# Kernel tuning notes

Measured on AMD Instinct MI355X. Metric: run time of the kernel, lower is better.

The kernel has to match this reference:

```python
import jax, jax.numpy as jnp
import numpy as np

X_CH, Y_CH, DIM, NUM_HEAD = 256, 512, 128, 4
H_DIM = DIM // NUM_HEAD
GAMMA = H_DIM ** (-0.5)


def conv1x1(x, w, b):
    # x: [B,C,H,W], w: [O,C], b: [O]
    return jnp.einsum('bchw,oc->bohw', x, w) + b[None, :, None, None]


def _split_qkv(qkv, bs, hw):
    # qkv: [B, 3*DIM, H, W] -> q,k,v each [B, NUM_HEAD, HW, H_DIM]
    qkv = qkv.reshape(bs, 3, NUM_HEAD, H_DIM, hw)
    qkv = jnp.transpose(qkv, (1, 0, 2, 4, 3))  # [3, B, H, HW, D]
    return qkv[0], qkv[1], qkv[2]


def setup_inputs() -> dict:
    key = jax.random.key(0)
    ks = jax.random.split(key, 12)
    s = lambda fan_in: 1.0 / np.sqrt(fan_in)
    x = jax.random.normal(ks[0], (2, X_CH, 64, 64), dtype=jnp.float32)
    y = jax.random.normal(ks[1], (2, Y_CH, 32, 32), dtype=jnp.float32)
    wx_qkv = jax.random.normal(ks[2], (3 * DIM, X_CH), dtype=jnp.float32) * s(X_CH)
    bx_qkv = jax.random.normal(ks[3], (3 * DIM,), dtype=jnp.float32) * s(X_CH)
    wy_qkv = jax.random.normal(ks[4], (3 * DIM, Y_CH), dtype=jnp.float32) * s(Y_CH)
    by_qkv = jax.random.normal(ks[5], (3 * DIM,), dtype=jnp.float32) * s(Y_CH)
    wpx = jax.random.normal(ks[6], (X_CH, DIM), dtype=jnp.float32) * s(DIM)
    bpx = jax.random.normal(ks[7], (X_CH,), dtype=jnp.float32) * s(DIM)
    wpy = jax.random.normal(ks[8], (Y_CH, DIM), dtype=jnp.float32) * s(DIM)
    bpy = jax.random.normal(ks[9], (Y_CH,), dtype=jnp.float32) * s(DIM)
    return {"x": x, "y": y, "wx_qkv": wx_qkv, "bx_qkv": bx_qkv,
            "wy_qkv": wy_qkv, "by_qkv": by_qkv,
            "wpx": wpx, "bpx": bpx, "wpy": wpy, "bpy": bpy}


def reference(x, y, wx_qkv, bx_qkv, wy_qkv, by_qkv, wpx, bpx, wpy, bpy):
    bs, _, h_x, w_x = x.shape
    _, _, h_y, w_y = y.shape
    hw_x, hw_y = h_x * w_x, h_y * w_y

    q_x, k_x, v_x = _split_qkv(conv1x1(x, wx_qkv, bx_qkv), bs, hw_x)
    q_y, k_y, v_y = _split_qkv(conv1x1(y, wy_qkv, by_qkv), bs, hw_y)

    # x attends to y
    atten_x = jax.nn.softmax(jnp.einsum('bhqd,bhkd->bhqk', q_x, k_y) * GAMMA, axis=-1)
    out_x = jnp.einsum('bhqk,bhkd->bhqd', atten_x, v_y)  # [B,H,HWx,D]
    out_x = jnp.transpose(out_x, (0, 1, 3, 2)).reshape(bs, DIM, h_x, w_x)

    # y attends to x
    atten_y = jax.nn.softmax(jnp.einsum('bhqd,bhkd->bhqk', q_y, k_x) * GAMMA, axis=-1)
    out_y = jnp.einsum('bhqk,bhkd->bhqd', atten_y, v_x)
    out_y = jnp.transpose(out_y, (0, 1, 3, 2)).reshape(bs, DIM, h_y, w_y)

    out_x = conv1x1(out_x, wpx, bpx) + x
    out_y = conv1x1(out_y, wpy, bpy) + y
    return out_x, out_y
```

## Files before the change

### kernel.cpp

```cpp
#include <hip/hip_runtime.h>
#include <hip/hip_bf16.h>
#include <cstdint>

#define B 2
#define NH 4
#define HD 32
#define DIM 128
#define CX 256
#define CY 512
#define PX 4096
#define PY 1024
#define QKV 384
#define GAMMA 0.17677669529663687f

typedef unsigned short u16;
typedef unsigned int u32;

using short8 = __attribute__((ext_vector_type(8))) short;
using f32x4  = __attribute__((ext_vector_type(4))) float;

__device__ __forceinline__ float bf2f(u32 h) {
  union { u32 u; float f; } v; v.u = (h & 0xffffu) << 16; return v.f;
}
__device__ __forceinline__ u16 f2bf(float f) {
  u32 u = __float_as_uint(f);
  u32 r = (u + 0x7fffu + ((u >> 16) & 1u)) >> 16;
  return (u16)r;
}
__device__ __forceinline__ void gl_lds16(const u16* g, u16* l) {
  __builtin_amdgcn_global_load_lds(
      (const __attribute__((address_space(1))) void*)g,
      (__attribute__((address_space(3))) void*)l, 16, 0, 0);
}
__device__ __forceinline__ bool is_f32(const void* src) {
  u32 u = ((const u16*)src)[2 * (threadIdx.x & 63)];
  return __ballot((u & 0x7F80u) >= 0x4600u) != 0ull;
}

#define N_X   (B * CX * PX)
#define N_Y   (B * CY * PY)
#define N_WX  (QKV * CX)
#define N_BX  (QKV)
#define N_WY  (QKV * CY)
#define N_BY  (QKV)
#define N_WPX (CX * DIM)
#define N_BPX (CX)
#define N_WPY (CY * DIM)
#define N_BPY (CY)

enum : size_t {
  OFF_CWX   = 0,
  OFF_CBX   = OFF_CWX  + N_WX,
  OFF_CWY   = OFF_CBX  + N_BX,
  OFF_CBY   = OFF_CWY  + N_WY,
  OFF_CWPX  = OFF_CBY  + N_BY,
  OFF_CBPX  = OFF_CWPX + N_WPX,
  OFF_CWPY  = OFF_CBPX + N_BPX,
  OFF_CBPY  = OFF_CWPY + N_WPY,
  OFF_XT    = OFF_CBPY + N_BPY,
  OFF_YT    = OFF_XT   + (size_t)B * PX * CX,
  OFF_QPX   = OFF_YT   + (size_t)B * PY * CY,
  OFF_KPX   = OFF_QPX  + (size_t)B * NH * PX * HD,
  OFF_QPY   = OFF_KPX  + (size_t)B * NH * PX * HD,
  OFF_KPY   = OFF_QPY  + (size_t)B * NH * PY * HD,
  OFF_VCX   = OFF_KPY  + (size_t)B * NH * PY * HD,
  OFF_VCY   = OFF_VCX  + (size_t)B * DIM * PX,
  OFF_OTX   = OFF_VCY  + (size_t)B * DIM * PY,
  OFF_OTY   = OFF_OTX  + (size_t)B * PX * DIM,
  WS_END    = OFF_OTY  + (size_t)B * PY * DIM,
};

#define XPX_BLKS 2048
#define XPY_BLKS 1024
__global__ __launch_bounds__(256) void k_prep(
    const void* x, const void* y, const void* wx, const void* bx,
    const void* wy, const void* by, const void* wpx, const void* bpx,
    const void* wpy, const void* bpy, u16* __restrict__ ws) {
  const int id = blockIdx.x;
  if (id < XPX_BLKS + XPY_BLKS) {
    __shared__ u16 tile[32][33];
    const void* src; u16* dst; int C, P, p_t, c_t, b;
    if (id < XPX_BLKS) {
      src = x; dst = ws + OFF_XT; C = CX; P = PX;
      p_t = id & 127; c_t = (id >> 7) & 7; b = id >> 10;
    } else {
      int id2 = id - XPX_BLKS;
      src = y; dst = ws + OFF_YT; C = CY; P = PY;
      p_t = id2 & 31; c_t = (id2 >> 5) & 15; b = id2 >> 9;
    }
    const bool f32in = is_f32(src);
    const int tx = threadIdx.x & 31, ty = threadIdx.x >> 5;
    const int p0 = p_t * 32, c0 = c_t * 32;
#pragma unroll
    for (int i = 0; i < 4; i++) {
      int cl = ty * 4 + i;
      size_t sidx = ((size_t)b * C + c0 + cl) * P + p0 + tx;
      u16 v = f32in ? f2bf(((const float*)src)[sidx]) : ((const u16*)src)[sidx];
      tile[cl][tx] = v;
    }
    __syncthreads();
#pragma unroll
    for (int i = 0; i < 4; i++) {
      int pl = ty * 4 + i;
      dst[((size_t)b * P + p0 + pl) * C + c0 + tx] = tile[tx][pl];
    }
  } else {
    int wid = id - (XPX_BLKS + XPY_BLKS);
    const void* src; size_t dstoff; int n, base;
    if      (wid < 48)  { src = wx;  dstoff = OFF_CWX;  n = N_WX;  base = 0; }
    else if (wid < 49)  { src = bx;  dstoff = OFF_CBX;  n = N_BX;  base = 48; }
    else if (wid < 145) { src = wy;  dstoff = OFF_CWY;  n = N_WY;  base = 49; }
    else if (wid < 146) { src = by;  dstoff = OFF_CBY;  n = N_BY;  base = 145; }
    else if (wid < 162) { src = wpx; dstoff = OFF_CWPX; n = N_WPX; base = 146; }
    else if (wid < 163) { src = bpx; dstoff = OFF_CBPX; n = N_BPX; base = 162; }
    else if (wid < 195) { src = wpy; dstoff = OFF_CWPY; n = N_WPY; base = 163; }
    else                { src = bpy; dstoff = OFF_CBPY; n = N_BPY; base = 195; }
    const bool f32in = is_f32(src);
    int e0 = (wid - base) * 2048 + threadIdx.x * 8;
    if (e0 >= n) return;
    u16* dst = ws + dstoff + e0;
    if (f32in) {
      const float* s = (const float*)src + e0;
      float4 a = *(const float4*)s;
      float4 bq = *(const float4*)(s + 4);
      ushort4 o0, o1;
      o0.x = f2bf(a.x);  o0.y = f2bf(a.y);  o0.z = f2bf(a.z);  o0.w = f2bf(a.w);
      o1.x = f2bf(bq.x); o1.y = f2bf(bq.y); o1.z = f2bf(bq.z); o1.w = f2bf(bq.w);
      *(ushort4*)dst = o0;
      *(ushort4*)(dst + 4) = o1;
    } else {
      uint4 v = *(const uint4*)((const u16*)src + e0);
      *(uint4*)dst = v;
    }
  }
}

__global__ __launch_bounds__(256) void k_qkv(u16* __restrict__ ws) {
  const int t = threadIdx.x;
  const int lane = t & 63, w = t >> 6;
  const int ql = lane & 15, quad = lane >> 4;
  const int b = blockIdx.z;

  const u16 *W, *Xt, *bias; u16 *qp, *kp, *vc; int C, P, pxb;
  if (blockIdx.x < 64) {
    W = ws + OFF_CWX; Xt = ws + OFF_XT; bias = ws + OFF_CBX;
    qp = ws + OFF_QPX; kp = ws + OFF_KPX; vc = ws + OFF_VCX;
    C = CX; P = PX; pxb = blockIdx.x;
  } else {
    W = ws + OFF_CWY; Xt = ws + OFF_YT; bias = ws + OFF_CBY;
    qp = ws + OFF_QPY; kp = ws + OFF_KPY; vc = ws + OFF_VCY;
    C = CY; P = PY; pxb = blockIdx.x - 64;
  }
  const int p_w = pxb * 64 + (w & 1) * 32;
  const int o_w = blockIdx.y * 64 + (w >> 1) * 32;

  const u16* wr0 = W + (size_t)(o_w + ql) * C;
  const u16* wr1 = W + (size_t)(o_w + 16 + ql) * C;
  const u16* xr0 = Xt + ((size_t)b * P + p_w + ql) * C;
  const u16* xr1 = Xt + ((size_t)b * P + p_w + 16 + ql) * C;

  union U { uint4 u; short8 s; };
  f32x4 acc[2][2];
#pragma unroll
  for (int i = 0; i < 2; i++)
#pragma unroll
    for (int j = 0; j < 2; j++) acc[i][j] = (f32x4){0.f, 0.f, 0.f, 0.f};

#pragma unroll 4
  for (int c0 = 0; c0 < C; c0 += 32) {
    int off = c0 + quad * 8;
    U a0, a1, b0, b1;
    a0.u = *(const uint4*)&wr0[off];
    a1.u = *(const uint4*)&wr1[off];
    b0.u = *(const uint4*)&xr0[off];
    b1.u = *(const uint4*)&xr1[off];
    acc[0][0] = __builtin_amdgcn_mfma_f32_16x16x32_bf16(a0.s, b0.s, acc[0][0], 0, 0, 0);
    acc[0][1] = __builtin_amdgcn_mfma_f32_16x16x32_bf16(a0.s, b1.s, acc[0][1], 0, 0, 0);
    acc[1][0] = __builtin_amdgcn_mfma_f32_16x16x32_bf16(a1.s, b0.s, acc[1][0], 0, 0, 0);
    acc[1][1] = __builtin_amdgcn_mfma_f32_16x16x32_bf16(a1.s, b1.s, acc[1][1], 0, 0, 0);
  }

  float bs[2][4];
#pragma unroll
  for (int oi = 0; oi < 2; oi++)
#pragma unroll
    for (int r = 0; r < 4; r++)
      bs[oi][r] = bf2f(bias[o_w + oi * 16 + quad * 4 + r]);

  if (blockIdx.y < 4) {
    bool isq = blockIdx.y < 2;
    float scale = isq ? GAMMA : 1.0f;
    u16* dstT = isq ? qp : kp;
#pragma unroll
    for (int oi = 0; oi < 2; oi++)
#pragma unroll
      for (int pi = 0; pi < 2; pi++) {
        int p = p_w + pi * 16 + ql;
        int o = o_w + oi * 16 + quad * 4 - (isq ? 0 : 128);
        int hh = o >> 5, d = o & 31;
        f32x4 a = acc[oi][pi];
        uint2 pk;
        pk.x = (u32)f2bf((a[0] + bs[oi][0]) * scale) |
               ((u32)f2bf((a[1] + bs[oi][1]) * scale) << 16);
        pk.y = (u32)f2bf((a[2] + bs[oi][2]) * scale) |
               ((u32)f2bf((a[3] + bs[oi][3]) * scale) << 16);
        *(uint2*)&dstT[((size_t)(b * NH + hh) * P + p) * HD + d] = pk;
      }
  } else {
#pragma unroll
    for (int oi = 0; oi < 2; oi++)
#pragma unroll
      for (int pi = 0; pi < 2; pi++) {
        int p = p_w + pi * 16 + ql;
        f32x4 a = acc[oi][pi];
#pragma unroll
        for (int r = 0; r < 4; r++) {
          int o = o_w + oi * 16 + quad * 4 + r - 256;
          vc[((size_t)b * DIM + o) * P + p] = f2bf(a[r] + bs[oi][r]);
        }
      }
  }
}

template <int NQF>
__device__ __forceinline__ void attn_core(
    const u16* __restrict__ Qp, const u16* __restrict__ Kp,
    const u16* __restrict__ Vc, u16* __restrict__ Ot, int Pq, int Pk,
    int q0, int h, int b, u16* pool, float (*mlb)[4][64]) {
  const int t = threadIdx.x;
  const int lane = t & 63, w = t >> 6;
  const int ql = lane & 15, quad = lane >> 4;

  union U { uint4 u; short8 s; };
  U qf[NQF];
#pragma unroll
  for (int qi = 0; qi < NQF; qi++)
    qf[qi].u = *(const uint4*)&Qp[((size_t)(b * NH + h) * Pq + q0 + qi * 16 + ql) * HD + quad * 8];

  const int kspan = Pk >> 2;
  const int kk0 = w * kspan;
  const int niter = kspan >> 5;

  const u16* gK0 = Kp + ((size_t)(b * NH + h) * Pk + kk0 + (lane & 31)) * HD + (lane >> 5) * 8;
  const u16* gK1 = gK0 + 16;
  const u16* gV0 = Vc + ((size_t)(b * DIM + h * HD + (lane & 15))) * Pk + kk0 + (lane >> 4) * 8;
  const u16* gV1 = gV0 + (size_t)16 * Pk;

  u16* wpool = pool + w * 4096;

  gl_lds16(gK0, wpool);
  gl_lds16(gK1, wpool + 512);
  gl_lds16(gV0, wpool + 2048);
  gl_lds16(gV1, wpool + 2048 + 512);

  const int f0 = ((ql >> 2) << 3) | (ql & 3);
  const int kA0 = (f0 + 32 * quad) * 8;
  const int kA1 = kA0 + 32;
  const int vA0 = 2048 + lane * 8;
  const int vA1 = 2048 + 512 + lane * 8;

  f32x4 o0[NQF], o1[NQF];
  float m_run[NQF], l_run[NQF];
#pragma unroll
  for (int qi = 0; qi < NQF; qi++) {
    o0[qi] = (f32x4){0.f, 0.f, 0.f, 0.f};
    o1[qi] = (f32x4){0.f, 0.f, 0.f, 0.f};
    m_run[qi] = -1e30f; l_run[qi] = 0.f;
  }

  int buf = 0;
  for (int it = 0; it < niter; it++) {
    if (it + 1 < niter) {
      size_t go = (size_t)(it + 1) * 32;
      u16* dst = wpool + (buf ^ 1) * 1024;
      gl_lds16(gK0 + go * HD, dst);
      gl_lds16(gK1 + go * HD, dst + 512);
      gl_lds16(gV0 + go, dst + 2048);
      gl_lds16(gV1 + go, dst + 2048 + 512);
      __builtin_amdgcn_sched_barrier(0);
      __builtin_amdgcn_s_waitcnt(0x0F74);
      __builtin_amdgcn_sched_barrier(0);
    } else {
      __builtin_amdgcn_sched_barrier(0);
      __builtin_amdgcn_s_waitcnt(0x0F70);
      __builtin_amdgcn_sched_barrier(0);
    }
    const u16* bb = wpool + buf * 1024;
    U ka, kb, va, vb;
    ka.u = *(const uint4*)&bb[kA0];
    kb.u = *(const uint4*)&bb[kA1];
    va.u = *(const uint4*)&bb[vA0];
    vb.u = *(const uint4*)&bb[vA1];

#pragma unroll
    for (int qi = 0; qi < NQF; qi++) {
      f32x4 z = {0.f, 0.f, 0.f, 0.f};
      f32x4 st0 = __builtin_amdgcn_mfma_f32_16x16x32_bf16(ka.s, qf[qi].s, z, 0, 0, 0);
      f32x4 st1 = __builtin_amdgcn_mfma_f32_16x16x32_bf16(kb.s, qf[qi].s, z, 0, 0, 0);

      float s[8] = {st0[0], st0[1], st0[2], st0[3], st1[0], st1[1], st1[2], st1[3]};
      float cm = fmaxf(fmaxf(fmaxf(s[0], s[1]), fmaxf(s[2], s[3])),
                       fmaxf(fmaxf(s[4], s[5]), fmaxf(s[6], s[7])));
      cm = fmaxf(cm, __shfl_xor(cm, 16));
      cm = fmaxf(cm, __shfl_xor(cm, 32));
      float m_new = fmaxf(m_run[qi], cm);
      float alpha = __expf(m_run[qi] - m_new);
      float p[8], ls = 0.f;
#pragma unroll
      for (int i = 0; i < 8; i++) { p[i] = __expf(s[i] - m_new); ls += p[i]; }
      ls += __shfl_xor(ls, 16);
      ls += __shfl_xor(ls, 32);
      l_run[qi] = l_run[qi] * alpha + ls;
      m_run[qi] = m_new;
#pragma unroll
      for (int r = 0; r < 4; r++) { o0[qi][r] *= alpha; o1[qi][r] *= alpha; }

      U pf;
      pf.u.x = (u32)f2bf(p[0]) | ((u32)f2bf(p[1]) << 16);
      pf.u.y = (u32)f2bf(p[2]) | ((u32)f2bf(p[3]) << 16);
      pf.u.z = (u32)f2bf(p[4]) | ((u32)f2bf(p[5]) << 16);
      pf.u.w = (u32)f2bf(p[6]) | ((u32)f2bf(p[7]) << 16);

      o0[qi] = __builtin_amdgcn_mfma_f32_16x16x32_bf16(va.s, pf.s, o0[qi], 0, 0, 0);
      o1[qi] = __builtin_amdgcn_mfma_f32_16x16x32_bf16(vb.s, pf.s, o1[qi], 0, 0, 0);
    }
    buf ^= 1;
  }

  float* Of = (float*)(pool + (size_t)w * 4096);
#pragma unroll
  for (int qi = 0; qi < NQF; qi++) {
#pragma unroll
    for (int r = 0; r < 4; r++) {
      Of[(qi * 16 + ql) * 32 + quad * 4 + r] = o0[qi][r];
      Of[(qi * 16 + ql) * 32 + 16 + quad * 4 + r] = o1[qi][r];
    }
    if (quad == 0) {
      mlb[0][w][qi * 16 + ql] = m_run[qi];
      mlb[1][w][qi * 16 + ql] = l_run[qi];
    }
  }
  __syncthreads();

  const float* OfA = (const float*)pool;
#pragma unroll
  for (int k = 0; k < NQF * 2; k++) {
    int e = t + k * 256;
    int q = e >> 5, d = e & 31;
    float m0 = mlb[0][0][q], m1 = mlb[0][1][q], m2 = mlb[0][2][q], m3 = mlb[0][3][q];
    float M = fmaxf(fmaxf(m0, m1), fmaxf(m2, m3));
    float c0 = __expf(m0 - M), c1 = __expf(m1 - M), c2 = __expf(m2 - M), c3 = __expf(m3 - M);
    float lt = c0 * mlb[1][0][q] + c1 * mlb[1][1][q] + c2 * mlb[1][2][q] + c3 * mlb[1][3][q];
    int di = q * 32 + d;
    float v = c0 * OfA[di] + c1 * OfA[2048 + di] +
              c2 * OfA[4096 + di] + c3 * OfA[6144 + di];
    Ot[((size_t)b * Pq + q0 + q) * DIM + h * HD + d] = f2bf(v / lt);
  }
}

__global__ __launch_bounds__(256) void k_attn(u16* __restrict__ ws) {
  __shared__ __align__(16) u16 pool[16384];
  __shared__ float mlb[2][4][64];
  const int h = blockIdx.y, b = blockIdx.z;
  if (blockIdx.x < 64) {
    attn_core<4>(ws + OFF_QPX, ws + OFF_KPY, ws + OFF_VCY, ws + OFF_OTX,
                 PX, PY, blockIdx.x * 64, h, b, pool, mlb);
  } else {
    attn_core<2>(ws + OFF_QPY, ws + OFF_KPX, ws + OFF_VCX, ws + OFF_OTY,
                 PY, PX, (blockIdx.x - 64) * 32, h, b, pool, mlb);
  }
}

__global__ __launch_bounds__(256) void k_proj(
    u16* __restrict__ ws, void* __restrict__ outv,
    const void* __restrict__ resx, const void* __restrict__ resy) {
  const u16 *W, *A, *bias; const void* res; int OT, P, pxb; size_t out_off;
  if (blockIdx.x < 64) {
    if (blockIdx.y >= 4) return;
    W = ws + OFF_CWPX; A = ws + OFF_OTX; bias = ws + OFF_CBPX;
    res = resx; OT = CX; P = PX; pxb = blockIdx.x; out_off = 0;
  } else {
    W = ws + OFF_CWPY; A = ws + OFF_OTY; bias = ws + OFF_CBPY;
    res = resy; OT = CY; P = PY; pxb = blockIdx.x - 64;
    out_off = (size_t)B * CX * PX;
  }
  const bool f32io = is_f32(res);
  const int t = threadIdx.x;
  const int lane = t & 63, w = t >> 6;
  const int ql = lane & 15, quad = lane >> 4;
  const int p_w = pxb * 64 + (w & 1) * 32;
  const int o_w = blockIdx.y * 64 + (w >> 1) * 32;
  const int b = blockIdx.z;

  const u16* wr0 = W + (size_t)(o_w + ql) * DIM;
  const u16* wr1 = W + (size_t)(o_w + 16 + ql) * DIM;
  const u16* xr0 = A + ((size_t)b * P + p_w + ql) * DIM;
  const u16* xr1 = A + ((size_t)b * P + p_w + 16 + ql) * DIM;

  union U { uint4 u; short8 s; };
  f32x4 acc[2][2];
#pragma unroll
  for (int i = 0; i < 2; i++)
#pragma unroll
    for (int j = 0; j < 2; j++) acc[i][j] = (f32x4){0.f, 0.f, 0.f, 0.f};

#pragma unroll
  for (int c0 = 0; c0 < DIM; c0 += 32) {
    int off = c0 + quad * 8;
    U a0, a1, b0, b1;
    a0.u = *(const uint4*)&wr0[off];
    a1.u = *(const uint4*)&wr1[off];
    b0.u = *(const uint4*)&xr0[off];
    b1.u = *(const uint4*)&xr1[off];
    acc[0][0] = __builtin_amdgcn_mfma_f32_16x16x32_bf16(a0.s, b0.s, acc[0][0], 0, 0, 0);
    acc[0][1] = __builtin_amdgcn_mfma_f32_16x16x32_bf16(a0.s, b1.s, acc[0][1], 0, 0, 0);
    acc[1][0] = __builtin_amdgcn_mfma_f32_16x16x32_bf16(a1.s, b0.s, acc[1][0], 0, 0, 0);
    acc[1][1] = __builtin_amdgcn_mfma_f32_16x16x32_bf16(a1.s, b1.s, acc[1][1], 0, 0, 0);
  }

#pragma unroll
  for (int oi = 0; oi < 2; oi++)
#pragma unroll
    for (int pi = 0; pi < 2; pi++) {
      int p = p_w + pi * 16 + ql;
      f32x4 a = acc[oi][pi];
#pragma unroll
      for (int r = 0; r < 4; r++) {
        int o = o_w + oi * 16 + quad * 4 + r;
        float bv = bf2f(bias[o]);
        size_t idx = ((size_t)b * OT + o) * P + p;
        float rv = f32io ? ((const float*)res)[idx] : bf2f(((const u16*)res)[idx]);
        float v = a[r] + bv + rv;
        if (f32io) ((float*)outv)[out_off + idx] = v;
        else       ((u16*)outv)[out_off + idx] = f2bf(v);
      }
    }
}

extern "C" void kernel_launch(void* const* d_in, const int* in_sizes, int n_in,
                              void* d_out, int out_size, void* d_ws, size_t ws_size,
                              hipStream_t stream) {
  (void)in_sizes; (void)n_in; (void)out_size; (void)ws_size;
  u16* ws = (u16*)d_ws;

  k_prep<<<dim3(XPX_BLKS + XPY_BLKS + 196), 256, 0, stream>>>(
      d_in[0], d_in[1], d_in[2], d_in[3], d_in[4], d_in[5],
      d_in[6], d_in[7], d_in[8], d_in[9], ws);
  k_qkv<<<dim3(80, 6, B), 256, 0, stream>>>(ws);
  k_attn<<<dim3(96, NH, B), 256, 0, stream>>>(ws);
  k_proj<<<dim3(80, 8, B), 256, 0, stream>>>(ws, d_out, d_in[0], d_in[1]);
}
```

Before: 163.0 us.

## Load K/V fragments directly to registers and truncate P to bf16 via perm

Replaces the global-to-LDS double-buffered staging of K and V tiles with direct global loads into registers, prefetched one iteration ahead. This removes LDS round trips and waitcnt barriers. Register pressure goes up and the loads are less coalesced. Separately, the round-to-nearest f32-to-bf16 conversion of the softmax probabilities is replaced by a byte-permute truncation, which saves ALU work but gives slightly less accurate rounding.

```diff
diff --git a/kernel.cpp b/kernel.cpp
--- a/kernel.cpp
+++ b/kernel.cpp
@@ -26,11 +26,6 @@
   u32 u = __float_as_uint(f);
   u32 r = (u + 0x7fffu + ((u >> 16) & 1u)) >> 16;
   return (u16)r;
-}
-__device__ __forceinline__ void gl_lds16(const u16* g, u16* l) {
-  __builtin_amdgcn_global_load_lds(
-      (const __attribute__((address_space(1))) void*)g,
-      (__attribute__((address_space(3))) void*)l, 16, 0, 0);
 }
 __device__ __forceinline__ bool is_f32(const void* src) {
   u32 u = ((const u16*)src)[2 * (threadIdx.x & 63)];
@@ -240,24 +235,17 @@
   const int kspan = Pk >> 2;
   const int kk0 = w * kspan;
   const int niter = kspan >> 5;
-
-  const u16* gK0 = Kp + ((size_t)(b * NH + h) * Pk + kk0 + (lane & 31)) * HD + (lane >> 5) * 8;
-  const u16* gK1 = gK0 + 16;
-  const u16* gV0 = Vc + ((size_t)(b * DIM + h * HD + (lane & 15))) * Pk + kk0 + (lane >> 4) * 8;
-  const u16* gV1 = gV0 + (size_t)16 * Pk;
-
-  u16* wpool = pool + w * 4096;
-
-  gl_lds16(gK0, wpool);
-  gl_lds16(gK1, wpool + 512);
-  gl_lds16(gV0, wpool + 2048);
-  gl_lds16(gV1, wpool + 2048 + 512);
-
   const int f0 = ((ql >> 2) << 3) | (ql & 3);
-  const int kA0 = (f0 + 32 * quad) * 8;
-  const int kA1 = kA0 + 32;
-  const int vA0 = 2048 + lane * 8;
-  const int vA1 = 2048 + 512 + lane * 8;
+
+  const u16* kbase = Kp + ((size_t)(b * NH + h) * Pk + kk0 + f0) * HD + quad * 8;
+  const u16* v0base = Vc + ((size_t)(b * DIM + h * HD + ql)) * Pk + kk0 + quad * 8;
+  const u16* v1base = v0base + (size_t)16 * Pk;
+
+  U ka, kb, va, vb, kan, kbn, van, vbn;
+  ka.u = *(const uint4*)&kbase[0];
+  kb.u = *(const uint4*)&kbase[4 * HD];
+  va.u = *(const uint4*)&v0base[0];
+  vb.u = *(const uint4*)&v1base[0];
 
   f32x4 o0[NQF], o1[NQF];
   float m_run[NQF], l_run[NQF];
@@ -268,29 +256,14 @@
     m_run[qi] = -1e30f; l_run[qi] = 0.f;
   }
 
-  int buf = 0;
   for (int it = 0; it < niter; it++) {
     if (it + 1 < niter) {
       size_t go = (size_t)(it + 1) * 32;
-      u16* dst = wpool + (buf ^ 1) * 1024;
-      gl_lds16(gK0 + go * HD, dst);
-      gl_lds16(gK1 + go * HD, dst + 512);
-      gl_lds16(gV0 + go, dst + 2048);
-      gl_lds16(gV1 + go, dst + 2048 + 512);
-      __builtin_amdgcn_sched_barrier(0);
-      __builtin_amdgcn_s_waitcnt(0x0F74);
-      __builtin_amdgcn_sched_barrier(0);
-    } else {
-      __builtin_amdgcn_sched_barrier(0);
-      __builtin_amdgcn_s_waitcnt(0x0F70);
-      __builtin_amdgcn_sched_barrier(0);
-    }
-    const u16* bb = wpool + buf * 1024;
-    U ka, kb, va, vb;
-    ka.u = *(const uint4*)&bb[kA0];
-    kb.u = *(const uint4*)&bb[kA1];
-    va.u = *(const uint4*)&bb[vA0];
-    vb.u = *(const uint4*)&bb[vA1];
+      kan.u = *(const uint4*)&kbase[go * HD];
+      kbn.u = *(const uint4*)&kbase[(go + 4) * HD];
+      van.u = *(const uint4*)&v0base[go];
+      vbn.u = *(const uint4*)&v1base[go];
+    }
 
 #pragma unroll
     for (int qi = 0; qi < NQF; qi++) {
@@ -316,15 +289,15 @@
       for (int r = 0; r < 4; r++) { o0[qi][r] *= alpha; o1[qi][r] *= alpha; }
 
       U pf;
-      pf.u.x = (u32)f2bf(p[0]) | ((u32)f2bf(p[1]) << 16);
-      pf.u.y = (u32)f2bf(p[2]) | ((u32)f2bf(p[3]) << 16);
-      pf.u.z = (u32)f2bf(p[4]) | ((u32)f2bf(p[5]) << 16);
-      pf.u.w = (u32)f2bf(p[6]) | ((u32)f2bf(p[7]) << 16);
+      pf.u.x = __builtin_amdgcn_perm(__float_as_uint(p[1]), __float_as_uint(p[0]), 0x07060302u);
+      pf.u.y = __builtin_amdgcn_perm(__float_as_uint(p[3]), __float_as_uint(p[2]), 0x07060302u);
+      pf.u.z = __builtin_amdgcn_perm(__float_as_uint(p[5]), __float_as_uint(p[4]), 0x07060302u);
+      pf.u.w = __builtin_amdgcn_perm(__float_as_uint(p[7]), __float_as_uint(p[6]), 0x07060302u);
 
       o0[qi] = __builtin_amdgcn_mfma_f32_16x16x32_bf16(va.s, pf.s, o0[qi], 0, 0, 0);
       o1[qi] = __builtin_amdgcn_mfma_f32_16x16x32_bf16(vb.s, pf.s, o1[qi], 0, 0, 0);
     }
-    buf ^= 1;
+    ka = kan; kb = kbn; va = van; vb = vbn;
   }
 
   float* Of = (float*)(pool + (size_t)w * 4096);
```

Measured after the change: 150.4 us. -7.8%, faster.
